# Kernel optimization log

Measured on AMD Instinct MI355X. Metric: run time of the kernel, lower is better.

Reference implementation:

```python
import jax, jax.numpy as jnp
import numpy as np

B, NORB, N_UP, N_DN, HIDDEN = 1024, 128, 32, 32, 4096


def setup_inputs() -> dict:
    rng = np.random.default_rng(0)
    # Build valid occupancy configs: exactly N_UP up-electrons (bit 0) and
    # N_DN down-electrons (bit 1) per sample. Encoding: 0=empty,1=up,2=dn,3=updn.
    up_order = np.argsort(rng.random((B, NORB)), axis=1)
    dn_order = np.argsort(rng.random((B, NORB)), axis=1)
    up_bit = np.zeros((B, NORB), np.int32)
    dn_bit = np.zeros((B, NORB), np.int32)
    np.put_along_axis(up_bit, up_order[:, :N_UP], 1, axis=1)
    np.put_along_axis(dn_bit, dn_order[:, :N_DN], 1, axis=1)
    x = jnp.asarray(up_bit + 2 * dn_bit, dtype=jnp.int32)

    key = jax.random.key(0)
    k1, k2, k3 = jax.random.split(key, 3)
    orbitals = jax.random.normal(k1, (NORB, N_UP), jnp.float32)
    W1 = jax.random.normal(k2, (4 * NORB, HIDDEN), jnp.float32) / np.sqrt(4 * NORB)
    b1 = jnp.zeros((HIDDEN,), jnp.float32)
    W2 = jax.random.normal(k3, (HIDDEN, NORB * N_UP), jnp.float32) / np.sqrt(HIDDEN)
    b2 = jnp.zeros((NORB * N_UP,), jnp.float32)
    return {"x": x, "orbitals": orbitals, "W1": W1, "b1": b1, "W2": W2, "b2": b2}


def _occupancies_to_electrons(x, n_up, n_dn):
    # Per-spin sorted positions of occupied orbitals. Stable argsort on the
    # inverted mask keeps occupied sites first, in ascending orbital order.
    up_mask = (x & 1) == 1
    dn_mask = (x & 2) == 2
    y_up = jnp.argsort(jnp.where(up_mask, 0, 1), axis=-1, stable=True)[:, :n_up]
    y_dn = jnp.argsort(jnp.where(dn_mask, 0, 1), axis=-1, stable=True)[:, :n_dn]
    return y_up, y_dn


def reference(x, orbitals, W1, b1, W2, b2):
    Bsz, norb = x.shape
    n_up = orbitals.shape[1]

    # correction_fun: MLP on one-hot config -> [B, norb, n_up]
    h = jax.nn.one_hot(x, 4, dtype=W1.dtype).reshape(Bsz, -1)  # [B, 4*norb]
    h = jax.nn.relu(h @ W1 + b1)                               # [B, hidden]
    corrections = (h @ W2 + b2).reshape(Bsz, norb, n_up)       # [B, norb, n_up]

    y_up, y_dn = _occupancies_to_electrons(x, n_up, n_up)
    y_up = y_up[..., None]  # [B, n_up, 1]
    y_dn = y_dn[..., None]

    # gather orbital rows + correction rows per electron (spin-symmetric orbitals)
    phi_up = jnp.take_along_axis(orbitals[None], y_up, axis=1)  # [B, n_up, n_up]
    phi_dn = jnp.take_along_axis(orbitals[None], y_dn, axis=1)
    d_up = jnp.take_along_axis(corrections, y_up, axis=1)
    d_dn = jnp.take_along_axis(corrections, y_dn, axis=1)

    s_up, log_det_up = jnp.linalg.slogdet(phi_up + d_up)
    s_dn, log_det_dn = jnp.linalg.slogdet(phi_dn + d_dn)
    return log_det_up + log_det_dn + jnp.log(s_up * s_dn + 0j)  # complex [B]
```

## Files before the change

kernel.cpp:

```cpp
#include <hip/hip_runtime.h>
#include <cmath>

#define B_SZ  1024
#define NORB  128
#define NUP   32
#define HID   4096
#define NCORR (NORB * NUP)
#define K1    (4 * NORB)

typedef short    bf16x8 __attribute__((ext_vector_type(8)));
typedef _Float16 f16x8  __attribute__((ext_vector_type(8)));
typedef float    f32x4  __attribute__((ext_vector_type(4)));

__device__ __forceinline__ unsigned short f2bf_rne(float f) {
    unsigned int u = __float_as_uint(f);
    u += 0x7FFFu + ((u >> 16) & 1u);
    return (unsigned short)(u >> 16);
}

__global__ __launch_bounds__(256) void k_pack(const float* __restrict__ W1,
                                              unsigned short* __restrict__ W1ph,
                                              unsigned short* __restrict__ W1pl,
                                              const float* __restrict__ W2,
                                              _Float16* __restrict__ Bh16,
                                              _Float16* __restrict__ Bl16) {
    __shared__ float tile[64][33];
    int bid = blockIdx.x;
    int t = threadIdx.x;

    int isW2 = (bid >= 1024);
    int i = isW2 ? bid - 1024 : bid;
    int n0 = (i & 127) * 32;
    int k0 = (i >> 7) * 64;
    const float* W = isW2 ? W2 : W1;

    int rl = t >> 3, c4 = (t & 7) * 4;
#pragma unroll
    for (int q = 0; q < 2; ++q) {
        int kl = rl + 32 * q;
        float4 v = *(const float4*)(W + (size_t)(k0 + kl) * 4096 + n0 + c4);
        tile[kl][c4 + 0] = v.x; tile[kl][c4 + 1] = v.y;
        tile[kl][c4 + 2] = v.z; tile[kl][c4 + 3] = v.w;
    }
    __syncthreads();

    int nl = t & 31, kg = t >> 5;
    int nt = (n0 + nl) >> 4;
    int kt = (k0 >> 5) + (kg >> 2);
    int lane_o = (kg & 3) * 16 + (nl & 15);

    if (isW2) {
        size_t o = (((size_t)nt * 128 + kt) * 64 + lane_o) * 8;
        f16x8 hi8, lo8;
#pragma unroll
        for (int j = 0; j < 8; ++j) {
            float v = tile[kg * 8 + j][nl];
            _Float16 hi = (_Float16)v;
            hi8[j] = hi;
            lo8[j] = (_Float16)((v - (float)hi) * 2048.0f);
        }
        *(f16x8*)(Bh16 + o) = hi8;
        *(f16x8*)(Bl16 + o) = lo8;
    } else {
        size_t o = (((size_t)nt * 16 + kt) * 64 + lane_o) * 8;
        unsigned short hi8[8], lo8[8];
#pragma unroll
        for (int j = 0; j < 8; ++j) {
            float v = tile[kg * 8 + j][nl];
            unsigned short hi = f2bf_rne(v);
            float fhi = __uint_as_float((unsigned int)hi << 16);
            hi8[j] = hi;
            lo8[j] = f2bf_rne(v - fhi);
        }
        *(bf16x8*)(W1ph + o) = *(bf16x8*)hi8;
        *(bf16x8*)(W1pl + o) = *(bf16x8*)lo8;
    }
}

__global__ __launch_bounds__(256, 2) void k_hidden3(const int* __restrict__ x,
                                                    const unsigned short* __restrict__ Bph,
                                                    const unsigned short* __restrict__ Bpl,
                                                    const float* __restrict__ b1,
                                                    _Float16* __restrict__ h16) {
    __shared__ unsigned int sxp[64][8];
    __shared__ unsigned short BF[2][4][4][512];
    __shared__ float Ht[64][132];

    int n0 = blockIdx.x * 128;
    int m0 = blockIdx.y * 64;
    int t = threadIdx.x;
    int w = t >> 6, lane = t & 63;
    int lm = lane & 15, kq = lane >> 4;
    int wn = w * 32;

#pragma unroll
    for (int i = 0; i < 2; ++i) {
        int id = t + 256 * i;
        int row = id >> 3, d = id & 7;
        const int* src = x + (size_t)(m0 + row) * NORB + d * 16;
        unsigned int dw = 0;
#pragma unroll
        for (int b = 0; b < 16; ++b) dw |= ((unsigned int)(src[b] & 3)) << (2 * b);
        sxp[row][d] = dw;
    }

    int nt0 = (n0 + wn) >> 4;
    const unsigned short* bh0 = Bph + (size_t)nt0 * (16 * 512) + (size_t)lane * 8;
    const unsigned short* bh1 = Bph + (size_t)(nt0 + 1) * (16 * 512) + (size_t)lane * 8;
    const unsigned short* bl0 = Bpl + (size_t)nt0 * (16 * 512) + (size_t)lane * 8;
    const unsigned short* bl1 = Bpl + (size_t)(nt0 + 1) * (16 * 512) + (size_t)lane * 8;

    f32x4 acc[4][2] = {};

    bf16x8 r0 = *(const bf16x8*)(bh0);
    bf16x8 r1 = *(const bf16x8*)(bh1);
    bf16x8 r2 = *(const bf16x8*)(bl0);
    bf16x8 r3 = *(const bf16x8*)(bl1);
    bf16x8 r4 = *(const bf16x8*)(bh0 + 512);
    bf16x8 r5 = *(const bf16x8*)(bh1 + 512);
    bf16x8 r6 = *(const bf16x8*)(bl0 + 512);
    bf16x8 r7 = *(const bf16x8*)(bl1 + 512);

    __syncthreads();

    for (int p = 0; p < 8; ++p) {
        if (p) __syncthreads();

        *(bf16x8*)&BF[0][w][0][lane * 8] = r0;
        *(bf16x8*)&BF[0][w][1][lane * 8] = r1;
        *(bf16x8*)&BF[0][w][2][lane * 8] = r2;
        *(bf16x8*)&BF[0][w][3][lane * 8] = r3;
        *(bf16x8*)&BF[1][w][0][lane * 8] = r4;
        *(bf16x8*)&BF[1][w][1][lane * 8] = r5;
        *(bf16x8*)&BF[1][w][2][lane * 8] = r6;
        *(bf16x8*)&BF[1][w][3][lane * 8] = r7;
        __syncthreads();

        int kn = (p + 1 < 8) ? p + 1 : 7;
        r0 = *(const bf16x8*)(bh0 + (2 * kn) * 512);
        r1 = *(const bf16x8*)(bh1 + (2 * kn) * 512);
        r2 = *(const bf16x8*)(bl0 + (2 * kn) * 512);
        r3 = *(const bf16x8*)(bl1 + (2 * kn) * 512);
        r4 = *(const bf16x8*)(bh0 + (2 * kn + 1) * 512);
        r5 = *(const bf16x8*)(bh1 + (2 * kn + 1) * 512);
        r6 = *(const bf16x8*)(bl0 + (2 * kn + 1) * 512);
        r7 = *(const bf16x8*)(bl1 + (2 * kn + 1) * 512);
        __builtin_amdgcn_sched_barrier(0);

#pragma unroll
        for (int s = 0; s < 2; ++s) {
            int kt = 2 * p + s;
            int i0 = kt * 8 + kq * 2;
            int dwIdx = i0 >> 4;
            int sh = (i0 & 15) * 2;
            bf16x8 af[4];
#pragma unroll
            for (int fm = 0; fm < 4; ++fm) {
                unsigned int dw = sxp[fm * 16 + lm][dwIdx];
                unsigned int c01 = (dw >> sh) & 0xFu;
                union { bf16x8 v; unsigned long long u[2]; } a;
                a.u[0] = 0x3F80ULL << ((c01 & 3u) * 16);
                a.u[1] = 0x3F80ULL << ((c01 >> 2) * 16);
                af[fm] = a.v;
            }

            bf16x8 b0h = *(const bf16x8*)&BF[s][w][0][lane * 8];
            bf16x8 b1h = *(const bf16x8*)&BF[s][w][1][lane * 8];
            bf16x8 b0l = *(const bf16x8*)&BF[s][w][2][lane * 8];
            bf16x8 b1l = *(const bf16x8*)&BF[s][w][3][lane * 8];

#pragma unroll
            for (int fm = 0; fm < 4; ++fm) {
                acc[fm][0] = __builtin_amdgcn_mfma_f32_16x16x32_bf16(af[fm], b0h, acc[fm][0], 0, 0, 0);
                acc[fm][0] = __builtin_amdgcn_mfma_f32_16x16x32_bf16(af[fm], b0l, acc[fm][0], 0, 0, 0);
                acc[fm][1] = __builtin_amdgcn_mfma_f32_16x16x32_bf16(af[fm], b1h, acc[fm][1], 0, 0, 0);
                acc[fm][1] = __builtin_amdgcn_mfma_f32_16x16x32_bf16(af[fm], b1l, acc[fm][1], 0, 0, 0);
            }
        }
    }

    __syncthreads();
#pragma unroll
    for (int fm = 0; fm < 4; ++fm)
#pragma unroll
        for (int fn = 0; fn < 2; ++fn) {
            int n = wn + fn * 16 + lm;
            float bv = b1[n0 + n];
#pragma unroll
            for (int r = 0; r < 4; ++r)
                Ht[fm * 16 + kq * 4 + r][n] = fmaxf(acc[fm][fn][r] + bv, 0.f);
        }
    __syncthreads();

    size_t mt0 = (size_t)(m0 >> 4), kt0 = (size_t)(n0 >> 5);
#pragma unroll
    for (int fi = 0; fi < 4; ++fi) {
        int f = w * 4 + fi;
        int mt = f >> 2, ktn = f & 3;
        int m = mt * 16 + lm;
        int kn = ktn * 32 + kq * 8;
        float4 v0 = *(const float4*)&Ht[m][kn];
        float4 v1 = *(const float4*)&Ht[m][kn + 4];
        float vv[8] = {v0.x, v0.y, v0.z, v0.w, v1.x, v1.y, v1.z, v1.w};
        f16x8 o16;
#pragma unroll
        for (int j = 0; j < 8; ++j) o16[j] = (_Float16)vv[j];
        size_t o = (((mt0 + mt) * 128 + (kt0 + ktn)) * 64 + lane) * 8;
        *(f16x8*)(h16 + o) = o16;
    }
}

__global__ __launch_bounds__(256) void k_hidden_f32(const int* __restrict__ x,
                                                    const float* __restrict__ W1,
                                                    const float* __restrict__ b1,
                                                    float* __restrict__ h) {
    int b = blockIdx.x, tid = threadIdx.x;
    __shared__ int sx[NORB];
    if (tid < NORB) sx[tid] = x[b * NORB + tid];
    __syncthreads();
    float acc[16];
#pragma unroll
    for (int u = 0; u < 16; ++u) acc[u] = b1[tid + 256 * u];
    for (int i = 0; i < NORB; ++i) {
        const float* row = W1 + (size_t)(4 * i + sx[i]) * HID;
#pragma unroll
        for (int u = 0; u < 16; ++u) acc[u] += row[tid + 256 * u];
    }
    float* hb = h + (size_t)b * HID;
#pragma unroll
    for (int u = 0; u < 16; ++u) hb[tid + 256 * u] = fmaxf(acc[u], 0.f);
}

__global__ __launch_bounds__(256, 2) void k_gemm7(const _Float16* __restrict__ Ap,
                                                  const _Float16* __restrict__ Bph,
                                                  const _Float16* __restrict__ Bpl,
                                                  const float* __restrict__ bias,
                                                  float* __restrict__ C) {
    __shared__ _Float16 AF[2][2][4][512];

    int bid = blockIdx.x;
    int lb = (bid & 7) * 64 + (bid >> 3);
    int local = lb & 63;
    int n0 = ((lb >> 6) * 4 + (local >> 4)) * 128;
    int m0 = (local & 15) * 64;

    int t = threadIdx.x;
    int w = t >> 6, lane = t & 63;
    int lm = lane & 15, kq = lane >> 4;
    int wn = w * 32;

    int mt0 = m0 >> 4;
    int nt0 = (n0 + wn) >> 4;

    const _Float16* ag  = Ap  + (size_t)(mt0 + w) * 65536 + (size_t)lane * 8;
    const _Float16* bh0 = Bph + (size_t)nt0 * 65536 + (size_t)lane * 8;
    const _Float16* bh1 = Bph + (size_t)(nt0 + 1) * 65536 + (size_t)lane * 8;
    const _Float16* bl0 = Bpl + (size_t)nt0 * 65536 + (size_t)lane * 8;
    const _Float16* bl1 = Bpl + (size_t)(nt0 + 1) * 65536 + (size_t)lane * 8;

    f32x4 accH[4][2] = {}, accL[4][2] = {};

    f16x8 r0 = *(const f16x8*)(ag);
    f16x8 r1 = *(const f16x8*)(ag + 512);
    f16x8 B0h0 = *(const f16x8*)(bh0);
    f16x8 B0h1 = *(const f16x8*)(bh1);
    f16x8 B0l0 = *(const f16x8*)(bl0);
    f16x8 B0l1 = *(const f16x8*)(bl1);
    f16x8 B1h0 = *(const f16x8*)(bh0 + 512);
    f16x8 B1h1 = *(const f16x8*)(bh1 + 512);
    f16x8 B1l0 = *(const f16x8*)(bl0 + 512);
    f16x8 B1l1 = *(const f16x8*)(bl1 + 512);

    for (int ktp = 0; ktp < 64; ++ktp) {
        int buf = ktp & 1;
        *(f16x8*)&AF[buf][0][w][lane * 8] = r0;
        *(f16x8*)&AF[buf][1][w][lane * 8] = r1;
        __syncthreads();

        int kn = (ktp + 1 < 64) ? ktp + 1 : 63;
        size_t o0 = (size_t)(2 * kn) * 512, o1 = o0 + 512;
        f16x8 nr0 = *(const f16x8*)(ag + o0);
        f16x8 nr1 = *(const f16x8*)(ag + o1);
        f16x8 nB0h0 = *(const f16x8*)(bh0 + o0);
        f16x8 nB0h1 = *(const f16x8*)(bh1 + o0);
        f16x8 nB0l0 = *(const f16x8*)(bl0 + o0);
        f16x8 nB0l1 = *(const f16x8*)(bl1 + o0);
        f16x8 nB1h0 = *(const f16x8*)(bh0 + o1);
        f16x8 nB1h1 = *(const f16x8*)(bh1 + o1);
        f16x8 nB1l0 = *(const f16x8*)(bl0 + o1);
        f16x8 nB1l1 = *(const f16x8*)(bl1 + o1);
        __builtin_amdgcn_sched_barrier(0);

        f16x8 a0[4], a1[4];
#pragma unroll
        for (int fm = 0; fm < 4; ++fm) {
            a0[fm] = *(const f16x8*)&AF[buf][0][fm][lane * 8];
            a1[fm] = *(const f16x8*)&AF[buf][1][fm][lane * 8];
        }

#pragma unroll
        for (int fm = 0; fm < 4; ++fm) {
            accH[fm][0] = __builtin_amdgcn_mfma_f32_16x16x32_f16(a0[fm], B0h0, accH[fm][0], 0, 0, 0);
            accL[fm][0] = __builtin_amdgcn_mfma_f32_16x16x32_f16(a0[fm], B0l0, accL[fm][0], 0, 0, 0);
            accH[fm][1] = __builtin_amdgcn_mfma_f32_16x16x32_f16(a0[fm], B0h1, accH[fm][1], 0, 0, 0);
            accL[fm][1] = __builtin_amdgcn_mfma_f32_16x16x32_f16(a0[fm], B0l1, accL[fm][1], 0, 0, 0);
        }
#pragma unroll
        for (int fm = 0; fm < 4; ++fm) {
            accH[fm][0] = __builtin_amdgcn_mfma_f32_16x16x32_f16(a1[fm], B1h0, accH[fm][0], 0, 0, 0);
            accL[fm][0] = __builtin_amdgcn_mfma_f32_16x16x32_f16(a1[fm], B1l0, accL[fm][0], 0, 0, 0);
            accH[fm][1] = __builtin_amdgcn_mfma_f32_16x16x32_f16(a1[fm], B1h1, accH[fm][1], 0, 0, 0);
            accL[fm][1] = __builtin_amdgcn_mfma_f32_16x16x32_f16(a1[fm], B1l1, accL[fm][1], 0, 0, 0);
        }

        r0 = nr0; r1 = nr1;
        B0h0 = nB0h0; B0h1 = nB0h1; B0l0 = nB0l0; B0l1 = nB0l1;
        B1h0 = nB1h0; B1h1 = nB1h1; B1l0 = nB1l0; B1l1 = nB1l1;
    }

    const float ls = 1.0f / 2048.0f;
#pragma unroll
    for (int fm = 0; fm < 4; ++fm)
#pragma unroll
        for (int fn = 0; fn < 2; ++fn) {
            int n = n0 + wn + fn * 16 + lm;
            float bv = bias[n];
#pragma unroll
            for (int r = 0; r < 4; ++r) {
                int m = m0 + fm * 16 + kq * 4 + r;
                C[(size_t)m * NCORR + n] = accH[fm][fn][r] + ls * accL[fm][fn][r] + bv;
            }
        }
}

#define BM 64
#define BN 64
#define BK 32
__global__ __launch_bounds__(256) void k_gemm(const float* __restrict__ A,
                                              const float* __restrict__ Bm,
                                              const float* __restrict__ bias,
                                              float* __restrict__ C) {
    __shared__ float As[BK][68];
    __shared__ float Bs[BK][BN];
    int n0 = blockIdx.x * BN, m0 = blockIdx.y * BM;
    int tid = threadIdx.x;
    int tm = tid >> 4, tn = tid & 15;
    int am = tid >> 3, ak = (tid & 7) * 4;
    int bk = tid >> 4, bn = (tid & 15) * 4;
    float acc[4][4] = {};
    for (int k0 = 0; k0 < HID; k0 += BK) {
#pragma unroll
        for (int s = 0; s < 2; ++s) {
            int m = am + 32 * s;
            float4 v = *(const float4*)(A + (size_t)(m0 + m) * HID + k0 + ak);
            As[ak + 0][m] = v.x; As[ak + 1][m] = v.y;
            As[ak + 2][m] = v.z; As[ak + 3][m] = v.w;
        }
#pragma unroll
        for (int s = 0; s < 2; ++s) {
            int k = bk + 16 * s;
            float4 v = *(const float4*)(Bm + (size_t)(k0 + k) * NCORR + n0 + bn);
            *(float4*)&Bs[k][bn] = v;
        }
        __syncthreads();
#pragma unroll
        for (int kk = 0; kk < BK; ++kk) {
            float4 a = *(const float4*)&As[kk][tm * 4];
            float4 bv = *(const float4*)&Bs[kk][tn * 4];
            float av[4] = {a.x, a.y, a.z, a.w};
            float bb[4] = {bv.x, bv.y, bv.z, bv.w};
#pragma unroll
            for (int i = 0; i < 4; ++i)
#pragma unroll
                for (int j = 0; j < 4; ++j) acc[i][j] += av[i] * bb[j];
        }
        __syncthreads();
    }
#pragma unroll
    for (int i = 0; i < 4; ++i) {
        int m = m0 + tm * 4 + i;
        float4 o;
        o.x = acc[i][0] + bias[n0 + tn * 4 + 0];
        o.y = acc[i][1] + bias[n0 + tn * 4 + 1];
        o.z = acc[i][2] + bias[n0 + tn * 4 + 2];
        o.w = acc[i][3] + bias[n0 + tn * 4 + 3];
        *(float4*)(C + (size_t)m * NCORR + n0 + tn * 4) = o;
    }
}

__global__ __launch_bounds__(128) void k_det(const int* __restrict__ x,
                                             const float* __restrict__ orbitals,
                                             const float* __restrict__ corr,
                                             float* __restrict__ out,
                                             int imag_off) {
    int b = blockIdx.x, tid = threadIdx.x;
    __shared__ int yup[NUP], ydn[NUP];
    __shared__ int cnt0[2];
    __shared__ float M[2][NUP][NUP + 1];
    __shared__ float rlog[2];
    __shared__ int rneg[2];

    int occ = x[b * NORB + tid];
    int lane0 = tid & 63;
    unsigned long long mup = __ballot(occ & 1);
    unsigned long long mdn = __ballot((occ >> 1) & 1);
    if (tid == 0) { cnt0[0] = __popcll(mup); cnt0[1] = __popcll(mdn); }
    __syncthreads();

    unsigned long long below = (1ull << lane0) - 1ull;
    int bu = (tid >= 64) ? cnt0[0] : 0;
    int bd = (tid >= 64) ? cnt0[1] : 0;
    if (occ & 1) yup[bu + __popcll(mup & below)] = tid;
    if (occ & 2) ydn[bd + __popcll(mdn & below)] = tid;
    __syncthreads();

    const float* cb = corr + (size_t)b * NCORR;
    for (int idx = tid; idx < 2 * NUP * NUP; idx += 128) {
        int s = idx >> 10;
        int i = (idx >> 5) & 31;
        int j = idx & 31;
        int r = s ? ydn[i] : yup[i];
        M[s][i][j] = orbitals[r * NUP + j] + cb[r * NUP + j];
    }
    __syncthreads();

    int wv = tid >> 6, lane = tid & 63;
    float (*Mm)[NUP + 1] = M[wv];
    float logdet = 0.f;
    int neg = 0;

    for (int k = 0; k < NUP; ++k) {
        float v = (lane >= k && lane < NUP) ? fabsf(Mm[lane][k]) : -1.f;
        int pi = lane;
#pragma unroll
        for (int off = 32; off > 0; off >>= 1) {
            float v2 = __shfl_down(v, off);
            int p2 = __shfl_down(pi, off);
            if (v2 > v) { v = v2; pi = p2; }
        }
        int p = __shfl(pi, 0);

        if (p != k) {
            if (lane < NUP) {
                float t1 = Mm[k][lane];
                Mm[k][lane] = Mm[p][lane];
                Mm[p][lane] = t1;
            }
            neg ^= 1;
        }
        __syncthreads();

        float pv = Mm[k][k];
        logdet += logf(fabsf(pv));
        if (pv < 0.f) neg ^= 1;

        int row = k + 1 + (lane & 31);
        int half = lane >> 5;
        if (row < NUP) {
            float f = Mm[row][k] / pv;
            for (int j = k + 1 + half; j < NUP; j += 2)
                Mm[row][j] -= f * Mm[k][j];
        }
        __syncthreads();
    }

    if (lane == 0) { rlog[wv] = logdet; rneg[wv] = neg; }
    __syncthreads();
    if (tid == 0) {
        out[b] = rlog[0] + rlog[1];
        if (imag_off > 0)
            out[imag_off + b] =
                (rneg[0] ^ rneg[1]) ? 3.14159265358979323846f : 0.f;
    }
}

extern "C" void kernel_launch(void* const* d_in, const int* in_sizes, int n_in,
                              void* d_out, int out_size, void* d_ws, size_t ws_size,
                              hipStream_t stream) {
    const int*   x        = (const int*)d_in[0];
    const float* orbitals = (const float*)d_in[1];
    const float* W1       = (const float*)d_in[2];
    const float* b1       = (const float*)d_in[3];
    const float* W2       = (const float*)d_in[4];
    const float* b2       = (const float*)d_in[5];
    float* out = (float*)d_out;
    int imag_off = (out_size == 2 * B_SZ) ? B_SZ : 0;

    const size_t need = (size_t)96 * 1024 * 1024;
    if (ws_size >= need) {
        _Float16* h16  = (_Float16*)d_ws;
        _Float16* Bh16 = h16 + (size_t)B_SZ * HID;
        _Float16* Bl16 = Bh16 + (size_t)HID * NCORR;
        float*    corr = (float*)(Bl16 + (size_t)HID * NCORR);

        unsigned short* W1ph = (unsigned short*)corr;
        unsigned short* W1pl = W1ph + (size_t)K1 * HID;

        k_pack<<<1024 + 8192, 256, 0, stream>>>(W1, W1ph, W1pl,
                                                W2, Bh16, Bl16);

        k_hidden3<<<dim3(HID / 128, B_SZ / 64), 256, 0, stream>>>(x, W1ph, W1pl, b1, h16);

        k_gemm7<<<512, 256, 0, stream>>>(h16, Bh16, Bl16, b2, corr);

        k_det<<<B_SZ, 128, 0, stream>>>(x, orbitals, corr, out, imag_off);
    } else {
        float* h    = (float*)d_ws;
        float* corr = h + (size_t)B_SZ * HID;
        k_hidden_f32<<<B_SZ, 256, 0, stream>>>(x, W1, b1, h);
        dim3 g2(NCORR / BN, B_SZ / BM);
        k_gemm<<<g2, 256, 0, stream>>>(h, W2, b2, corr);
        k_det<<<B_SZ, 128, 0, stream>>>(x, orbitals, corr, out, imag_off);
    }
}
```

Baseline: 235.9 us.

## Enlarge GEMM block tile to 128x128 and drop B register prefetch

```diff
diff --git a/kernel.cpp b/kernel.cpp
--- a/kernel.cpp
+++ b/kernel.cpp
@@ -231,19 +231,15 @@
     for (int u = 0; u < 16; ++u) hb[tid + 256 * u] = fmaxf(acc[u], 0.f);
 }
 
-__global__ __launch_bounds__(256, 2) void k_gemm7(const _Float16* __restrict__ Ap,
-                                                  const _Float16* __restrict__ Bph,
-                                                  const _Float16* __restrict__ Bpl,
-                                                  const float* __restrict__ bias,
-                                                  float* __restrict__ C) {
-    __shared__ _Float16 AF[2][2][4][512];
-
-    int bid = blockIdx.x;
-    int lb = (bid & 7) * 64 + (bid >> 3);
-    int local = lb & 63;
-    int n0 = ((lb >> 6) * 4 + (local >> 4)) * 128;
-    int m0 = (local & 15) * 64;
-
+__global__ __launch_bounds__(256, 2) void k_gemm13(const _Float16* __restrict__ Ap,
+                                                   const _Float16* __restrict__ Bph,
+                                                   const _Float16* __restrict__ Bpl,
+                                                   const float* __restrict__ bias,
+                                                   float* __restrict__ C) {
+    __shared__ _Float16 AF[2][2][8][512];
+
+    int n0 = blockIdx.x * 128;
+    int m0 = blockIdx.y * 128;
     int t = threadIdx.x;
     int w = t >> 6, lane = t & 63;
     int lm = lane & 15, kq = lane >> 4;
@@ -252,83 +248,76 @@
     int mt0 = m0 >> 4;
     int nt0 = (n0 + wn) >> 4;
 
-    const _Float16* ag  = Ap  + (size_t)(mt0 + w) * 65536 + (size_t)lane * 8;
+    const _Float16* ag0 = Ap + (size_t)(mt0 + 2 * w) * 65536 + (size_t)lane * 8;
+    const _Float16* ag1 = ag0 + 65536;
     const _Float16* bh0 = Bph + (size_t)nt0 * 65536 + (size_t)lane * 8;
     const _Float16* bh1 = Bph + (size_t)(nt0 + 1) * 65536 + (size_t)lane * 8;
     const _Float16* bl0 = Bpl + (size_t)nt0 * 65536 + (size_t)lane * 8;
     const _Float16* bl1 = Bpl + (size_t)(nt0 + 1) * 65536 + (size_t)lane * 8;
 
-    f32x4 accH[4][2] = {}, accL[4][2] = {};
-
-    f16x8 r0 = *(const f16x8*)(ag);
-    f16x8 r1 = *(const f16x8*)(ag + 512);
-    f16x8 B0h0 = *(const f16x8*)(bh0);
-    f16x8 B0h1 = *(const f16x8*)(bh1);
-    f16x8 B0l0 = *(const f16x8*)(bl0);
-    f16x8 B0l1 = *(const f16x8*)(bl1);
-    f16x8 B1h0 = *(const f16x8*)(bh0 + 512);
-    f16x8 B1h1 = *(const f16x8*)(bh1 + 512);
-    f16x8 B1l0 = *(const f16x8*)(bl0 + 512);
-    f16x8 B1l1 = *(const f16x8*)(bl1 + 512);
+    f32x4 accH[8][2] = {}, accL[8][2] = {};
+
+    f16x8 r00 = *(const f16x8*)(ag0);
+    f16x8 r01 = *(const f16x8*)(ag0 + 512);
+    f16x8 r10 = *(const f16x8*)(ag1);
+    f16x8 r11 = *(const f16x8*)(ag1 + 512);
 
     for (int ktp = 0; ktp < 64; ++ktp) {
         int buf = ktp & 1;
-        *(f16x8*)&AF[buf][0][w][lane * 8] = r0;
-        *(f16x8*)&AF[buf][1][w][lane * 8] = r1;
+        *(f16x8*)&AF[buf][0][2 * w + 0][lane * 8] = r00;
+        *(f16x8*)&AF[buf][1][2 * w + 0][lane * 8] = r01;
+        *(f16x8*)&AF[buf][0][2 * w + 1][lane * 8] = r10;
+        *(f16x8*)&AF[buf][1][2 * w + 1][lane * 8] = r11;
         __syncthreads();
 
         int kn = (ktp + 1 < 64) ? ktp + 1 : 63;
-        size_t o0 = (size_t)(2 * kn) * 512, o1 = o0 + 512;
-        f16x8 nr0 = *(const f16x8*)(ag + o0);
-        f16x8 nr1 = *(const f16x8*)(ag + o1);
-        f16x8 nB0h0 = *(const f16x8*)(bh0 + o0);
-        f16x8 nB0h1 = *(const f16x8*)(bh1 + o0);
-        f16x8 nB0l0 = *(const f16x8*)(bl0 + o0);
-        f16x8 nB0l1 = *(const f16x8*)(bl1 + o0);
-        f16x8 nB1h0 = *(const f16x8*)(bh0 + o1);
-        f16x8 nB1h1 = *(const f16x8*)(bh1 + o1);
-        f16x8 nB1l0 = *(const f16x8*)(bl0 + o1);
-        f16x8 nB1l1 = *(const f16x8*)(bl1 + o1);
+        size_t po0 = (size_t)(2 * kn) * 512, po1 = po0 + 512;
+        f16x8 nr00 = *(const f16x8*)(ag0 + po0);
+        f16x8 nr01 = *(const f16x8*)(ag0 + po1);
+        f16x8 nr10 = *(const f16x8*)(ag1 + po0);
+        f16x8 nr11 = *(const f16x8*)(ag1 + po1);
+        size_t o0 = (size_t)(2 * ktp) * 512, o1 = o0 + 512;
+        f16x8 B0h0 = *(const f16x8*)(bh0 + o0);
+        f16x8 B0h1 = *(const f16x8*)(bh1 + o0);
+        f16x8 B0l0 = *(const f16x8*)(bl0 + o0);
+        f16x8 B0l1 = *(const f16x8*)(bl1 + o0);
+        f16x8 B1h0 = *(const f16x8*)(bh0 + o1);
+        f16x8 B1h1 = *(const f16x8*)(bh1 + o1);
+        f16x8 B1l0 = *(const f16x8*)(bl0 + o1);
+        f16x8 B1l1 = *(const f16x8*)(bl1 + o1);
         __builtin_amdgcn_sched_barrier(0);
 
-        f16x8 a0[4], a1[4];
-#pragma unroll
-        for (int fm = 0; fm < 4; ++fm) {
-            a0[fm] = *(const f16x8*)&AF[buf][0][fm][lane * 8];
-            a1[fm] = *(const f16x8*)&AF[buf][1][fm][lane * 8];
-        }
-
-#pragma unroll
-        for (int fm = 0; fm < 4; ++fm) {
-            accH[fm][0] = __builtin_amdgcn_mfma_f32_16x16x32_f16(a0[fm], B0h0, accH[fm][0], 0, 0, 0);
-            accL[fm][0] = __builtin_amdgcn_mfma_f32_16x16x32_f16(a0[fm], B0l0, accL[fm][0], 0, 0, 0);
-            accH[fm][1] = __builtin_amdgcn_mfma_f32_16x16x32_f16(a0[fm], B0h1, accH[fm][1], 0, 0, 0);
-            accL[fm][1] = __builtin_amdgcn_mfma_f32_16x16x32_f16(a0[fm], B0l1, accL[fm][1], 0, 0, 0);
-        }
-#pragma unroll
-        for (int fm = 0; fm < 4; ++fm) {
-            accH[fm][0] = __builtin_amdgcn_mfma_f32_16x16x32_f16(a1[fm], B1h0, accH[fm][0], 0, 0, 0);
-            accL[fm][0] = __builtin_amdgcn_mfma_f32_16x16x32_f16(a1[fm], B1l0, accL[fm][0], 0, 0, 0);
-            accH[fm][1] = __builtin_amdgcn_mfma_f32_16x16x32_f16(a1[fm], B1h1, accH[fm][1], 0, 0, 0);
-            accL[fm][1] = __builtin_amdgcn_mfma_f32_16x16x32_f16(a1[fm], B1l1, accL[fm][1], 0, 0, 0);
-        }
-
-        r0 = nr0; r1 = nr1;
-        B0h0 = nB0h0; B0h1 = nB0h1; B0l0 = nB0l0; B0l1 = nB0l1;
-        B1h0 = nB1h0; B1h1 = nB1h1; B1l0 = nB1l0; B1l1 = nB1l1;
+#pragma unroll
+        for (int fm = 0; fm < 8; ++fm) {
+            f16x8 a = *(const f16x8*)&AF[buf][0][fm][lane * 8];
+            accH[fm][0] = __builtin_amdgcn_mfma_f32_16x16x32_f16(a, B0h0, accH[fm][0], 0, 0, 0);
+            accL[fm][0] = __builtin_amdgcn_mfma_f32_16x16x32_f16(a, B0l0, accL[fm][0], 0, 0, 0);
+            accH[fm][1] = __builtin_amdgcn_mfma_f32_16x16x32_f16(a, B0h1, accH[fm][1], 0, 0, 0);
+            accL[fm][1] = __builtin_amdgcn_mfma_f32_16x16x32_f16(a, B0l1, accL[fm][1], 0, 0, 0);
+        }
+#pragma unroll
+        for (int fm = 0; fm < 8; ++fm) {
+            f16x8 a = *(const f16x8*)&AF[buf][1][fm][lane * 8];
+            accH[fm][0] = __builtin_amdgcn_mfma_f32_16x16x32_f16(a, B1h0, accH[fm][0], 0, 0, 0);
+            accL[fm][0] = __builtin_amdgcn_mfma_f32_16x16x32_f16(a, B1l0, accL[fm][0], 0, 0, 0);
+            accH[fm][1] = __builtin_amdgcn_mfma_f32_16x16x32_f16(a, B1h1, accH[fm][1], 0, 0, 0);
+            accL[fm][1] = __builtin_amdgcn_mfma_f32_16x16x32_f16(a, B1l1, accL[fm][1], 0, 0, 0);
+        }
+
+        r00 = nr00; r01 = nr01; r10 = nr10; r11 = nr11;
     }
 
     const float ls = 1.0f / 2048.0f;
 #pragma unroll
-    for (int fm = 0; fm < 4; ++fm)
+    for (int fm = 0; fm < 8; ++fm)
 #pragma unroll
         for (int fn = 0; fn < 2; ++fn) {
             int n = n0 + wn + fn * 16 + lm;
             float bv = bias[n];
 #pragma unroll
-            for (int r = 0; r < 4; ++r) {
-                int m = m0 + fm * 16 + kq * 4 + r;
-                C[(size_t)m * NCORR + n] = accH[fm][fn][r] + ls * accL[fm][fn][r] + bv;
+            for (int rr = 0; rr < 4; ++rr) {
+                int m = m0 + fm * 16 + kq * 4 + rr;
+                C[(size_t)m * NCORR + n] = accH[fm][fn][rr] + ls * accL[fm][fn][rr] + bv;
             }
         }
 }
@@ -501,7 +490,8 @@
 
         k_hidden3<<<dim3(HID / 128, B_SZ / 64), 256, 0, stream>>>(x, W1ph, W1pl, b1, h16);
 
-        k_gemm7<<<512, 256, 0, stream>>>(h16, Bh16, Bl16, b2, corr);
+        dim3 g2(NCORR / 128, B_SZ / 128);
+        k_gemm13<<<g2, 256, 0, stream>>>(h16, Bh16, Bl16, b2, corr);
 
         k_det<<<B_SZ, 128, 0, stream>>>(x, orbitals, corr, out, imag_off);
     } else {
```

Measured after the change: 263.0 us. 11.5% more time.
